# Performance work log

Measured on AMD Instinct MI355X. Metric: run time of the kernel, lower is better.

## Reference

```python
import jax, jax.numpy as jnp
import numpy as np

B, S, D, H = 2, 2048, 1024, 16
HD = D // H  # head_dim = 64
LN_EPS = 1e-5


def setup_inputs() -> dict:
    key = jax.random.key(0)
    ks = jax.random.split(key, 14)
    w = 0.02  # weight init scale
    return {
        "q": jax.random.normal(ks[0], (B, S, D), jnp.float32),
        "k": jax.random.normal(ks[1], (B, S, D), jnp.float32),
        "v": jax.random.normal(ks[2], (B, S, D), jnp.float32),
        "mask": jnp.zeros((B, 1, S, S), dtype=bool),
        "training": 0,
        "wq_w": jax.random.normal(ks[3], (D, D), jnp.float32) * w,
        "wq_b": jnp.zeros((D,), jnp.float32),
        "wk_w": jax.random.normal(ks[4], (D, D), jnp.float32) * w,
        "wk_b": jnp.zeros((D,), jnp.float32),
        "wv_w": jax.random.normal(ks[5], (D, D), jnp.float32) * w,
        "wv_b": jnp.zeros((D,), jnp.float32),
        "wo_w": jax.random.normal(ks[6], (D, D), jnp.float32) * w,
        "wo_b": jnp.zeros((D,), jnp.float32),
        "ln_g": jnp.ones((D,), jnp.float32),
        "ln_b": jnp.zeros((D,), jnp.float32),
    }


def _linear(x, w, b):
    # torch nn.Linear: x @ W.T + b, W is [out, in]
    return jnp.einsum('bsd,od->bso', x, w) + b


def _split_heads(x):
    b, s, _ = x.shape
    return x.reshape(b, s, H, HD).transpose(0, 2, 1, 3)  # [B,H,S,HD]


def reference(q, k, v, mask, training, wq_w, wq_b, wk_w, wk_b, wv_w, wv_b,
              wo_w, wo_b, ln_g, ln_b):
    residual = q
    Q = _split_heads(_linear(q, wq_w, wq_b))
    K = _split_heads(_linear(k, wk_w, wk_b))
    V = _split_heads(_linear(v, wv_w, wv_b))
    # source computes sqrt(dk) in float16, then adds 1e-8
    dk = jnp.sqrt(jnp.asarray(HD, jnp.float16)).astype(jnp.float32) + 1e-8
    score = jnp.einsum('bhqd,bhkd->bhqk', Q, K) / dk  # [B,H,S,S]
    # NOTE: source applies NO softmax; masked score is used directly.
    attn = jnp.where(mask, -jnp.inf, score)
    ctx = jnp.einsum('bhqk,bhkd->bhqd', attn, V)  # [B,H,S,HD]
    b, _, s, _ = ctx.shape
    ctx = ctx.transpose(0, 2, 1, 3).reshape(b, s, D)  # [B,S,D]
    o = _linear(ctx, wo_w, wo_b)
    # dropout is identity in eval mode
    x = residual + o
    mu = jnp.mean(x, axis=-1, keepdims=True)
    var = jnp.mean(jnp.square(x - mu), axis=-1, keepdims=True)
    return ln_g * (x - mu) * jax.lax.rsqrt(var + LN_EPS) + ln_b
```

## Files before the change

### kernel.cpp

```cpp
#include <hip/hip_runtime.h>


typedef __bf16 bf16;
typedef __bf16 bf16x8 __attribute__((ext_vector_type(8)));
typedef float f32x4 __attribute__((ext_vector_type(4)));

#define MFMA16(a, b, c) __builtin_amdgcn_mfma_f32_16x16x32_bf16(a, b, c, 0, 0, 0)
#define BARRIER() asm volatile("s_barrier" ::: "memory")
#define VMCNT4() asm volatile("s_waitcnt vmcnt(4)" ::: "memory")
#define VMCNT0() asm volatile("s_waitcnt vmcnt(0)" ::: "memory")
#define LGKM0()                                        \
  do {                                                 \
    asm volatile("s_waitcnt lgkmcnt(0)" ::: "memory"); \
    __builtin_amdgcn_sched_barrier(0);                 \
  } while (0)

__device__ __forceinline__ bf16x8 ld8(const bf16* p) { return *(const bf16x8*)p; }

__device__ __forceinline__ void gload16(const void* g, void* l) {
  __builtin_amdgcn_global_load_lds((__attribute__((address_space(1))) void*)(g),
                                   (__attribute__((address_space(3))) void*)(l), 16, 0, 0);
}

__device__ __forceinline__ int swz4(int row) { return (row ^ (row >> 2)) & 3; }

__device__ __forceinline__ bf16x8 cvt8(f32x4 lo, f32x4 hi) {
  bf16x8 o;
  o[0] = (bf16)lo[0]; o[1] = (bf16)lo[1]; o[2] = (bf16)lo[2]; o[3] = (bf16)lo[3];
  o[4] = (bf16)hi[0]; o[5] = (bf16)hi[1]; o[6] = (bf16)hi[2]; o[7] = (bf16)hi[3];
  return o;
}

__device__ __forceinline__ void compute16(const char* buf, const int aoff[4], const int boff[4],
                                          f32x4 (&acc)[4][4]) {
  bf16x8 av[4], bv[4];
#pragma unroll
  for (int i = 0; i < 4; i++) av[i] = *(const bf16x8*)(buf + aoff[i]);
#pragma unroll
  for (int j = 0; j < 4; j++) bv[j] = *(const bf16x8*)(buf + boff[j]);
  __builtin_amdgcn_s_setprio(1);
#pragma unroll
  for (int i = 0; i < 4; i++)
#pragma unroll
    for (int j = 0; j < 4; j++) acc[i][j] = MFMA16(av[i], bv[j], acc[i][j]);
  __builtin_amdgcn_s_setprio(0);
}

__device__ __forceinline__ void ring128(const bf16* __restrict__ A, const bf16* __restrict__ B,
                                        char* lds, f32x4 (&acc)[4][4]) {
  const int t = threadIdx.x;
  const int lane = t & 63, wid = t >> 6;
  const int wr = wid >> 1, wc = wid & 1;
  const int r16 = lane & 15, kg = lane >> 4;

  int aoff[4], boff[4];
#pragma unroll
  for (int i = 0; i < 4; i++) {
    int row = wr * 64 + i * 16 + r16;
    aoff[i] = row * 64 + ((kg ^ swz4(row)) << 4);
    row = wc * 64 + i * 16 + r16;
    boff[i] = 8192 + row * 64 + ((kg ^ swz4(row)) << 4);
  }

  const int r1 = t >> 2, c = t & 3, r2 = r1 + 64;
  const bf16* pa1 = A + (size_t)r1 * 1024 + (c ^ swz4(r1)) * 8;
  const bf16* pa2 = A + (size_t)r2 * 1024 + (c ^ swz4(r2)) * 8;
  const bf16* pb1 = B + (size_t)r1 * 1024 + (c ^ swz4(r1)) * 8;
  const bf16* pb2 = B + (size_t)r2 * 1024 + (c ^ swz4(r2)) * 8;
  const int d1 = wid << 10, d2 = 4096 + (wid << 10);

#pragma unroll
  for (int p = 0; p < 2; p++) {
    char* d = lds + p * 16384;
    gload16(pa1 + p * 32, d + d1);
    gload16(pa2 + p * 32, d + d2);
    gload16(pb1 + p * 32, d + 8192 + d1);
    gload16(pb2 + p * 32, d + 8192 + d2);
  }
  pa1 += 64; pa2 += 64; pb1 += 64; pb2 += 64;

  int cb = 0, rb = 2;
  for (int kt = 0; kt < 30; kt++) {
    VMCNT4();
    BARRIER();
    {
      char* d = lds + rb * 16384;
      gload16(pa1, d + d1);
      gload16(pa2, d + d2);
      gload16(pb1, d + 8192 + d1);
      gload16(pb2, d + 8192 + d2);
      pa1 += 32; pa2 += 32; pb1 += 32; pb2 += 32;
    }
    compute16(lds + cb * 16384, aoff, boff, acc);
    LGKM0();
    cb = (cb == 2) ? 0 : cb + 1;
    rb = (rb == 2) ? 0 : rb + 1;
  }
  VMCNT4(); BARRIER();
  compute16(lds + cb * 16384, aoff, boff, acc);
  LGKM0();
  cb = (cb == 2) ? 0 : cb + 1;
  VMCNT0(); BARRIER();
  compute16(lds + cb * 16384, aoff, boff, acc);
}

__device__ __forceinline__ void proj_epi(f32x4 (&acc)[4][4], const float* bias,
                                         bf16* __restrict__ C, int m0, int n0) {
  const int lane = threadIdx.x & 63, wid = threadIdx.x >> 6;
  const int wr = wid >> 1, wc = wid & 1, r16 = lane & 15, kg = lane >> 4;
#pragma unroll
  for (int j = 0; j < 4; j++) {
    const int col = n0 + wc * 64 + j * 16 + r16;
    const float bj = bias[col];
#pragma unroll
    for (int i = 0; i < 4; i++) {
      const int row = m0 + wr * 64 + i * 16 + kg * 4;
#pragma unroll
      for (int r = 0; r < 4; r++)
        C[(size_t)(row + r) * 1024 + col] = (bf16)(acc[i][j][r] + bj);
    }
  }
}

__global__ __launch_bounds__(256) void cvt_kvw_kernel(
    const float* __restrict__ k, const float* __restrict__ v,
    const float* __restrict__ wk, const float* __restrict__ wv,
    bf16* __restrict__ kv_bf, bf16* __restrict__ wkv_bf, float* __restrict__ Mz) {
  const int bid = blockIdx.x;
  if (bid >= 5120) {
    float* p = Mz + (size_t)(bid - 5120) * 2048 + threadIdx.x * 8;
    *(f32x4*)p = f32x4{0.f, 0.f, 0.f, 0.f};
    *(f32x4*)(p + 4) = f32x4{0.f, 0.f, 0.f, 0.f};
    return;
  }
  const float* s; bf16* d; size_t dof; int x;
  if (bid < 4096) {
    const int y = bid >> 11; x = bid & 2047;
    s = (y == 0) ? k : v;
    d = kv_bf; dof = (size_t)y * 4194304u;
  } else {
    const int idx = bid - 4096; const int y = idx >> 9; x = idx & 511;
    s = (y == 0) ? wk : wv;
    d = wkv_bf; dof = (size_t)y * 1048576u;
  }
  const size_t i = ((size_t)x * 256 + threadIdx.x) * 8;
  *(bf16x8*)(d + dof + i) = cvt8(*(const f32x4*)(s + i), *(const f32x4*)(s + i + 4));
}

__global__ __launch_bounds__(256, 3) void fat_a_kernel(
    const bf16* __restrict__ kv_bf, const bf16* __restrict__ wkv_bf,
    const float* __restrict__ bk, const float* __restrict__ bv, bf16* __restrict__ KV_out,
    const float* __restrict__ q, const float* __restrict__ wq,
    bf16* __restrict__ q_bf, bf16* __restrict__ wq_bf) {
  __shared__ __align__(1024) char lds[49152];
  const int wg = blockIdx.x;
  if (wg < 512) {
    const int swz = (wg & 7) * 64 + (wg >> 3);
    const int mt = swz >> 3, nt = swz & 7;
    const int m0 = mt * 128, n0 = nt * 128;
    const int z = mt >> 5;
    f32x4 acc[4][4] = {};
    ring128(kv_bf + (size_t)m0 * 1024, wkv_bf + (size_t)z * 1048576u + (size_t)n0 * 1024,
            lds, acc);
    proj_epi(acc, z == 0 ? bk : bv, KV_out, m0, n0);
    return;
  }
  const int idx = wg - 512;
  const float* s; bf16* d; int x;
  if (idx < 2048) { s = q; d = q_bf; x = idx; }
  else            { s = wq; d = wq_bf; x = idx - 2048; }
  const size_t i = ((size_t)x * 256 + threadIdx.x) * 8;
  *(bf16x8*)(d + i) = cvt8(*(const f32x4*)(s + i), *(const f32x4*)(s + i + 4));
}

__global__ __launch_bounds__(256, 3) void fat_b_kernel(
    const bf16* __restrict__ q_bf, const bf16* __restrict__ wq_bf,
    const float* __restrict__ bq, bf16* __restrict__ Q_bf,
    const bf16* __restrict__ Kb, const bf16* __restrict__ Vb, float* __restrict__ M) {
  __shared__ __align__(1024) char lds[49152];
  const int wg = blockIdx.x;
  if (wg < 256) {
    const int swz = (wg & 7) * 32 + (wg >> 3);
    const int mt = swz >> 3, nt = swz & 7;
    const int m0 = mt * 128, n0 = nt * 128;
    f32x4 acc[4][4] = {};
    ring128(q_bf + (size_t)m0 * 1024, wq_bf + (size_t)n0 * 1024, lds, acc);
    proj_epi(acc, bq, Q_bf, m0, n0);
    return;
  }
  bf16 (*Kl)[136] = (bf16(*)[136])lds;
  bf16 (*Vl)[136] = (bf16(*)[136])(lds + 17408);
  const int bid = wg - 256;
  const int bh = bid >> 3, sc = bid & 7;
  const int b = bh >> 4, h = bh & 15;
  const int t = threadIdx.x;
  const int l = t & 63, w = t >> 6;
  const int r16 = l & 15, kg = l >> 4;
  f32x4 acc[4] = {};
  for (int sub = 0; sub < 2; ++sub) {
    const int s0 = sc * 256 + sub * 128;
    const size_t base = ((size_t)b * 2048 + s0) * 1024 + h * 64;
    if (sub) __syncthreads();
#pragma unroll
    for (int p = 0; p < 4; p++) {
      const int chunk = p * 256 + t;
      const int s = chunk >> 3, d0 = (chunk & 7) * 8;
      bf16x8 kv = ld8(Kb + base + (size_t)s * 1024 + d0);
      bf16x8 vv = ld8(Vb + base + (size_t)s * 1024 + d0);
#pragma unroll
      for (int e = 0; e < 8; e++) { Kl[d0 + e][s] = kv[e]; Vl[d0 + e][s] = vv[e]; }
    }
    __syncthreads();
#pragma unroll
    for (int ks = 0; ks < 4; ks++) {
      bf16x8 a = ld8(&Kl[w * 16 + r16][ks * 32 + kg * 8]);
#pragma unroll
      for (int j = 0; j < 4; j++) {
        bf16x8 bvv = ld8(&Vl[j * 16 + r16][ks * 32 + kg * 8]);
        acc[j] = MFMA16(a, bvv, acc[j]);
      }
    }
  }
  float* Mh = M + (size_t)bh * 4096;
#pragma unroll
  for (int j = 0; j < 4; j++)
#pragma unroll
    for (int r = 0; r < 4; r++)
      atomicAdd(&Mh[(w * 16 + kg * 4 + r) * 64 + j * 16 + r16], acc[j][r]);
}

__global__ __launch_bounds__(256) void gt_kernel(
    const float* __restrict__ Wo, const float* __restrict__ M, bf16* __restrict__ Gt) {
  const int bid = blockIdx.x;
  const int b = bid >> 7, h = (bid >> 3) & 15, nt = bid & 7;
  const int n0 = nt * 128;
  const float* Mh = M + (size_t)((b << 4) + h) * 4096;
  const int l = threadIdx.x & 63, w = threadIdx.x >> 6;
  const int r16 = l & 15, kg = l >> 4;
  f32x4 acc[2][4] = {};
#pragma unroll
  for (int kk = 0; kk < 2; kk++) {
    bf16x8 a[2];
#pragma unroll
    for (int i = 0; i < 2; i++) {
      const float* wp = Wo + (size_t)(n0 + w * 32 + i * 16 + r16) * 1024 + h * 64 + kk * 32 + kg * 8;
      a[i] = cvt8(*(const f32x4*)wp, *(const f32x4*)(wp + 4));
    }
#pragma unroll
    for (int j = 0; j < 4; j++) {
      const float* mp = Mh + (j * 16 + r16) * 64 + kk * 32 + kg * 8;
      f32x4 m0v = *(const f32x4*)mp;
      f32x4 m1v = *(const f32x4*)(mp + 4);
      f32x4 sl = {m0v[0] * 0.125f, m0v[1] * 0.125f, m0v[2] * 0.125f, m0v[3] * 0.125f};
      f32x4 sh = {m1v[0] * 0.125f, m1v[1] * 0.125f, m1v[2] * 0.125f, m1v[3] * 0.125f};
      bf16x8 bv = cvt8(sl, sh);
#pragma unroll
      for (int i = 0; i < 2; i++) acc[i][j] = MFMA16(a[i], bv, acc[i][j]);
    }
  }
  bf16* G = Gt + (size_t)b * 1048576u;
#pragma unroll
  for (int i = 0; i < 2; i++)
#pragma unroll
    for (int j = 0; j < 4; j++)
#pragma unroll
      for (int r = 0; r < 4; r++)
        G[(size_t)(n0 + w * 32 + i * 16 + kg * 4 + r) * 1024 + h * 64 + j * 16 + r16] =
            (bf16)acc[i][j][r];
}

__global__ __launch_bounds__(256, 3) void gemm_out_r(
    const bf16* __restrict__ Q, const bf16* __restrict__ Gt,
    const float* __restrict__ bo, const float* __restrict__ resid, bf16* __restrict__ xb) {
  __shared__ __align__(1024) char lds[49152];
  const int wg = blockIdx.x;
  const int swz = (wg & 7) * 32 + (wg >> 3);
  const int mt = swz >> 3, nt = swz & 7;
  const int m0 = mt * 128, n0 = nt * 128;

  f32x4 acc[4][4] = {};
  ring128(Q + (size_t)m0 * 1024, Gt + (size_t)(m0 >> 11) * 1048576u + (size_t)n0 * 1024, lds, acc);

  const int lane = threadIdx.x & 63, wid = threadIdx.x >> 6;
  const int wr = wid >> 1, wc = wid & 1, r16 = lane & 15, kg = lane >> 4;
#pragma unroll
  for (int j = 0; j < 4; j++) {
    const int col = n0 + wc * 64 + j * 16 + r16;
    const float bj = bo[col];
#pragma unroll
    for (int i = 0; i < 4; i++) {
      const int row = m0 + wr * 64 + i * 16 + kg * 4;
#pragma unroll
      for (int r = 0; r < 4; r++) {
        const size_t off = (size_t)(row + r) * 1024 + col;
        xb[off] = (bf16)(acc[i][j][r] + bj + resid[off]);
      }
    }
  }
}

__global__ __launch_bounds__(256) void ln_kernel(
    const bf16* __restrict__ xb, const float* __restrict__ g, const float* __restrict__ bb,
    float* __restrict__ out) {
  const int lane = threadIdx.x & 63, wid = threadIdx.x >> 6;
  const int row = (blockIdx.x << 2) + wid;
  const bf16* xr = xb + (size_t)row * 1024;
  bf16x8 h0 = ld8(xr + lane * 16);
  bf16x8 h1 = ld8(xr + lane * 16 + 8);
  float v[16];
#pragma unroll
  for (int e = 0; e < 8; e++) { v[e] = (float)h0[e]; v[8 + e] = (float)h1[e]; }
  float s = 0.f, s2 = 0.f;
#pragma unroll
  for (int e = 0; e < 16; e++) { s += v[e]; s2 += v[e] * v[e]; }
#pragma unroll
  for (int m = 32; m; m >>= 1) { s += __shfl_xor(s, m); s2 += __shfl_xor(s2, m); }
  const float mu = s * (1.0f / 1024.0f);
  const float rstd = rsqrtf(s2 * (1.0f / 1024.0f) - mu * mu + 1e-5f);
  float* orow = out + (size_t)row * 1024 + lane * 16;
#pragma unroll
  for (int e = 0; e < 4; e++) {
    f32x4 gg = *(const f32x4*)(g + lane * 16 + e * 4);
    f32x4 bv = *(const f32x4*)(bb + lane * 16 + e * 4);
    f32x4 o;
#pragma unroll
    for (int u = 0; u < 4; u++) o[u] = gg[u] * ((v[e * 4 + u] - mu) * rstd) + bv[u];
    *(f32x4*)(orow + e * 4) = o;
  }
}

extern "C" void kernel_launch(void* const* d_in, const int* in_sizes, int n_in,
                              void* d_out, int out_size, void* d_ws, size_t ws_size,
                              hipStream_t stream) {
  (void)in_sizes; (void)n_in; (void)out_size; (void)ws_size;
  const float* q    = (const float*)d_in[0];
  const float* k    = (const float*)d_in[1];
  const float* v    = (const float*)d_in[2];
  const float* wq_w = (const float*)d_in[5];
  const float* wq_b = (const float*)d_in[6];
  const float* wk_w = (const float*)d_in[7];
  const float* wk_b = (const float*)d_in[8];
  const float* wv_w = (const float*)d_in[9];
  const float* wv_b = (const float*)d_in[10];
  const float* wo_w = (const float*)d_in[11];
  const float* wo_b = (const float*)d_in[12];
  const float* ln_g = (const float*)d_in[13];
  const float* ln_b = (const float*)d_in[14];
  float* out = (float*)d_out;

  bf16* wsb    = (bf16*)d_ws;
  bf16* q_bf   = wsb;
  bf16* kv_bf  = wsb + 4194304u;
  bf16* w_bf   = wsb + 12582912u;
  bf16* QKV_bf = wsb + 15728640u;
  float* M     = (float*)(wsb + 28311552u);
  bf16* Gt     = wsb;
  bf16* xb     = wsb + 2097152u;

  cvt_kvw_kernel<<<5184, 256, 0, stream>>>(k, v, wk_w, wv_w, kv_bf, w_bf + 1048576u, M);
  fat_a_kernel<<<3072, 256, 0, stream>>>(kv_bf, w_bf + 1048576u, wk_b, wv_b,
                                         QKV_bf + 4194304u, q, wq_w, q_bf, w_bf);
  fat_b_kernel<<<512, 256, 0, stream>>>(q_bf, w_bf, wq_b, QKV_bf,
                                        QKV_bf + 4194304u, QKV_bf + 8388608u, M);
  gt_kernel<<<256, 256, 0, stream>>>(wo_w, M, Gt);
  gemm_out_r<<<256, 256, 0, stream>>>(QKV_bf, Gt, wo_b, q, xb);
  ln_kernel<<<1024, 256, 0, stream>>>(xb, ln_g, ln_b, out);
}
```

Before: 90.95 us.

## Fuse K^T V reduction into K/V projection epilogue and merge Gt into fat_b

New measurement: 91.97 us. Within noise of the previous version (+1.1%).

```diff
diff --git a/kernel.cpp b/kernel.cpp
--- a/kernel.cpp
+++ b/kernel.cpp
@@ -2,6 +2,7 @@
 
 
 typedef __bf16 bf16;
+typedef __bf16 bf16x4 __attribute__((ext_vector_type(4)));
 typedef __bf16 bf16x8 __attribute__((ext_vector_type(8)));
 typedef float f32x4 __attribute__((ext_vector_type(4)));
 
@@ -147,25 +148,73 @@
   *(bf16x8*)(d + dof + i) = cvt8(*(const f32x4*)(s + i), *(const f32x4*)(s + i + 4));
 }
 
-__global__ __launch_bounds__(256, 3) void fat_a_kernel(
-    const bf16* __restrict__ kv_bf, const bf16* __restrict__ wkv_bf,
-    const float* __restrict__ bk, const float* __restrict__ bv, bf16* __restrict__ KV_out,
+__global__ __launch_bounds__(256, 2) void fat_a_kernel(
+    const bf16* __restrict__ kv_bf, const bf16* __restrict__ wkv,
+    const float* __restrict__ bk, const float* __restrict__ bv_, float* __restrict__ Mout,
     const float* __restrict__ q, const float* __restrict__ wq,
     bf16* __restrict__ q_bf, bf16* __restrict__ wq_bf) {
   __shared__ __align__(1024) char lds[49152];
   const int wg = blockIdx.x;
-  if (wg < 512) {
-    const int swz = (wg & 7) * 64 + (wg >> 3);
+  if (wg < 256) {
+    const int swz = (wg & 7) * 32 + (wg >> 3);
     const int mt = swz >> 3, nt = swz & 7;
     const int m0 = mt * 128, n0 = nt * 128;
-    const int z = mt >> 5;
-    f32x4 acc[4][4] = {};
-    ring128(kv_bf + (size_t)m0 * 1024, wkv_bf + (size_t)z * 1048576u + (size_t)n0 * 1024,
-            lds, acc);
-    proj_epi(acc, z == 0 ? bk : bv, KV_out, m0, n0);
+    const int b = mt >> 4;
+
+    f32x4 accK[4][4] = {}, accV[4][4] = {};
+    ring128(kv_bf + (size_t)m0 * 1024, wkv + (size_t)n0 * 1024, lds, accK);
+    __syncthreads();
+    ring128(kv_bf + 4194304u + (size_t)m0 * 1024, wkv + 1048576u + (size_t)n0 * 1024,
+            lds, accV);
+    __syncthreads();
+
+    bf16 (*Kl)[136] = (bf16(*)[136])lds;
+    bf16 (*Vl)[136] = (bf16(*)[136])(lds + 17408);
+    const int lane = threadIdx.x & 63, wid = threadIdx.x >> 6;
+    const int wr = wid >> 1, wc = wid & 1, r16 = lane & 15, kg = lane >> 4;
+#pragma unroll
+    for (int g = 0; g < 2; ++g) {
+      if (g) __syncthreads();
+      if (wc == g) {
+#pragma unroll
+        for (int j = 0; j < 4; j++) {
+          const int col = n0 + g * 64 + j * 16 + r16;
+          const float bkj = bk[col], bvj = bv_[col];
+#pragma unroll
+          for (int i = 0; i < 4; i++) {
+            const int sb = wr * 64 + i * 16 + kg * 4;
+            bf16x4 pk, pv;
+#pragma unroll
+            for (int r = 0; r < 4; r++) {
+              pk[r] = (bf16)(accK[i][j][r] + bkj);
+              pv[r] = (bf16)(accV[i][j][r] + bvj);
+            }
+            *(bf16x4*)&Kl[j * 16 + r16][sb] = pk;
+            *(bf16x4*)&Vl[j * 16 + r16][sb] = pv;
+          }
+        }
+      }
+      __syncthreads();
+      f32x4 accm[4] = {};
+#pragma unroll
+      for (int ks = 0; ks < 4; ks++) {
+        bf16x8 a = ld8(&Kl[wid * 16 + r16][ks * 32 + kg * 8]);
+#pragma unroll
+        for (int j = 0; j < 4; j++) {
+          bf16x8 bb = ld8(&Vl[j * 16 + r16][ks * 32 + kg * 8]);
+          accm[j] = MFMA16(a, bb, accm[j]);
+        }
+      }
+      float* Mh = Mout + (size_t)(b * 16 + nt * 2 + g) * 4096;
+#pragma unroll
+      for (int j = 0; j < 4; j++)
+#pragma unroll
+        for (int r = 0; r < 4; r++)
+          atomicAdd(&Mh[(wid * 16 + kg * 4 + r) * 64 + j * 16 + r16], accm[j][r]);
+    }
     return;
   }
-  const int idx = wg - 512;
+  const int idx = wg - 256;
   const float* s; bf16* d; int x;
   if (idx < 2048) { s = q; d = q_bf; x = idx; }
   else            { s = wq; d = wq_bf; x = idx - 2048; }
@@ -176,7 +225,7 @@
 __global__ __launch_bounds__(256, 3) void fat_b_kernel(
     const bf16* __restrict__ q_bf, const bf16* __restrict__ wq_bf,
     const float* __restrict__ bq, bf16* __restrict__ Q_bf,
-    const bf16* __restrict__ Kb, const bf16* __restrict__ Vb, float* __restrict__ M) {
+    const float* __restrict__ Wo, const float* __restrict__ M, bf16* __restrict__ Gt) {
   __shared__ __align__(1024) char lds[49152];
   const int wg = blockIdx.x;
   if (wg < 256) {
@@ -188,50 +237,7 @@
     proj_epi(acc, bq, Q_bf, m0, n0);
     return;
   }
-  bf16 (*Kl)[136] = (bf16(*)[136])lds;
-  bf16 (*Vl)[136] = (bf16(*)[136])(lds + 17408);
   const int bid = wg - 256;
-  const int bh = bid >> 3, sc = bid & 7;
-  const int b = bh >> 4, h = bh & 15;
-  const int t = threadIdx.x;
-  const int l = t & 63, w = t >> 6;
-  const int r16 = l & 15, kg = l >> 4;
-  f32x4 acc[4] = {};
-  for (int sub = 0; sub < 2; ++sub) {
-    const int s0 = sc * 256 + sub * 128;
-    const size_t base = ((size_t)b * 2048 + s0) * 1024 + h * 64;
-    if (sub) __syncthreads();
-#pragma unroll
-    for (int p = 0; p < 4; p++) {
-      const int chunk = p * 256 + t;
-      const int s = chunk >> 3, d0 = (chunk & 7) * 8;
-      bf16x8 kv = ld8(Kb + base + (size_t)s * 1024 + d0);
-      bf16x8 vv = ld8(Vb + base + (size_t)s * 1024 + d0);
-#pragma unroll
-      for (int e = 0; e < 8; e++) { Kl[d0 + e][s] = kv[e]; Vl[d0 + e][s] = vv[e]; }
-    }
-    __syncthreads();
-#pragma unroll
-    for (int ks = 0; ks < 4; ks++) {
-      bf16x8 a = ld8(&Kl[w * 16 + r16][ks * 32 + kg * 8]);
-#pragma unroll
-      for (int j = 0; j < 4; j++) {
-        bf16x8 bvv = ld8(&Vl[j * 16 + r16][ks * 32 + kg * 8]);
-        acc[j] = MFMA16(a, bvv, acc[j]);
-      }
-    }
-  }
-  float* Mh = M + (size_t)bh * 4096;
-#pragma unroll
-  for (int j = 0; j < 4; j++)
-#pragma unroll
-    for (int r = 0; r < 4; r++)
-      atomicAdd(&Mh[(w * 16 + kg * 4 + r) * 64 + j * 16 + r16], acc[j][r]);
-}
-
-__global__ __launch_bounds__(256) void gt_kernel(
-    const float* __restrict__ Wo, const float* __restrict__ M, bf16* __restrict__ Gt) {
-  const int bid = blockIdx.x;
   const int b = bid >> 7, h = (bid >> 3) & 15, nt = bid & 7;
   const int n0 = nt * 128;
   const float* Mh = M + (size_t)((b << 4) + h) * 4096;
@@ -352,17 +358,15 @@
   bf16* q_bf   = wsb;
   bf16* kv_bf  = wsb + 4194304u;
   bf16* w_bf   = wsb + 12582912u;
-  bf16* QKV_bf = wsb + 15728640u;
+  bf16* Q_bf   = wsb + 15728640u;
+  bf16* Gt     = wsb + 19922944u;
+  bf16* xb     = wsb + 22020096u;
   float* M     = (float*)(wsb + 28311552u);
-  bf16* Gt     = wsb;
-  bf16* xb     = wsb + 2097152u;
 
   cvt_kvw_kernel<<<5184, 256, 0, stream>>>(k, v, wk_w, wv_w, kv_bf, w_bf + 1048576u, M);
-  fat_a_kernel<<<3072, 256, 0, stream>>>(kv_bf, w_bf + 1048576u, wk_b, wv_b,
-                                         QKV_bf + 4194304u, q, wq_w, q_bf, w_bf);
-  fat_b_kernel<<<512, 256, 0, stream>>>(q_bf, w_bf, wq_b, QKV_bf,
-                                        QKV_bf + 4194304u, QKV_bf + 8388608u, M);
-  gt_kernel<<<256, 256, 0, stream>>>(wo_w, M, Gt);
-  gemm_out_r<<<256, 256, 0, stream>>>(QKV_bf, Gt, wo_b, q, xb);
+  fat_a_kernel<<<2816, 256, 0, stream>>>(kv_bf, w_bf + 1048576u, wk_b, wv_b, M,
+                                         q, wq_w, q_bf, w_bf);
+  fat_b_kernel<<<512, 256, 0, stream>>>(q_bf, w_bf, wq_b, Q_bf, wo_w, M, Gt);
+  gemm_out_r<<<256, 256, 0, stream>>>(Q_bf, Gt, wo_b, q, xb);
   ln_kernel<<<1024, 256, 0, stream>>>(xb, ln_g, ln_b, out);
 }
```
